# Kernel tuning notes

Hardware: AMD Instinct MI355X
Metric: run time of the kernel (lower is better)

Reference implementation:

```python
import jax, jax.numpy as jnp
import numpy as np

N_NODES = 100000
N_EDGES = 1600000
D_FEAT = 48


def sage_conv(x, src, dst, Wl, Wr, b):
    # mean aggregation of neighbor messages x[src] at dst (PyG source_to_target)
    msg_sum = jax.ops.segment_sum(x[src], dst, num_segments=N_NODES)  # [N, d]
    cnt = jax.ops.segment_sum(jnp.ones((src.shape[0],), x.dtype), dst,
                              num_segments=N_NODES)  # [N]
    mean = msg_sum / jnp.maximum(cnt, 1.0)[:, None]
    # out = lin_l(mean neighbors) + lin_r(self); bias only on lin_l (PyG default)
    return mean @ Wl + b + x @ Wr


def setup_inputs() -> dict:
    key = jax.random.key(0)
    ks = jax.random.split(key, 8)
    x = jax.random.normal(ks[0], (N_NODES, D_FEAT), jnp.float32)
    edge_index = jax.random.randint(ks[1], (2, N_EDGES), 0, N_NODES, jnp.int64)
    def w(k, fi, fo):
        return jax.random.normal(k, (fi, fo), jnp.float32) / np.sqrt(fi)
    return {
        "x": x,
        "edge_index": edge_index,
        "W1l": w(ks[2], D_FEAT, 32), "W1r": w(ks[3], D_FEAT, 32),
        "b1": jnp.zeros((32,), jnp.float32),
        "W2l": w(ks[4], 32, 16), "W2r": w(ks[5], 32, 16),
        "b2": jnp.zeros((16,), jnp.float32),
        "Wlin": w(ks[6], 16, 2), "blin": jnp.zeros((2,), jnp.float32),
    }


def reference(x, edge_index, W1l, W1r, b1, W2l, W2r, b2, Wlin, blin):
    src, dst = edge_index[0], edge_index[1]
    h = jax.nn.relu(sage_conv(x, src, dst, W1l, W1r, b1))
    h = jax.nn.relu(sage_conv(h, src, dst, W2l, W2r, b2))
    return h @ Wlin + blin  # [N, 2] logits
```

## Files before the change

### kernel.cpp

```cpp
#include <hip/hip_runtime.h>
#include <hip/hip_bf16.h>


constexpr int NN  = 100000;
constexpr int NE  = 1600000;
constexpr int NCH = (NN + 255) / 256;
constexpr int NB  = 391;
constexpr int CAP = 4608;
constexpr int SEG = CAP + 3 * 256;
constexpr int T1  = 2048;
constexpr int EPT = T1 / 256;
constexpr int NB1 = (NE + T1 - 1) / T1;

__device__ __forceinline__ float bl(unsigned u) { return __uint_as_float(u << 16); }
__device__ __forceinline__ float bh(unsigned u) { return __uint_as_float(u & 0xffff0000u); }
__device__ __forceinline__ unsigned f2b(float x) {
    unsigned u = __float_as_uint(x);
    return (u + 0x7fffu + ((u >> 16) & 1u)) >> 16;
}
__device__ __forceinline__ unsigned pack2(float a, float b) {
    return f2b(a) | (f2b(b) << 16);
}

__device__ __forceinline__ int wave_incl_scan(int v, int lane) {
#pragma unroll
    for (int d = 1; d < 64; d <<= 1) {
        int t = __shfl_up(v, d, 64);
        if (lane >= d) v += t;
    }
    return v;
}

__global__ __launch_bounds__(256) void k1_kernel(
    const float* __restrict__ X,
    const float* __restrict__ Wl,
    const float* __restrict__ Wr,
    const int*   __restrict__ ei,
    int* __restrict__ bsize, unsigned* __restrict__ bbuf,
    __hip_bfloat16* __restrict__ P, __hip_bfloat16* __restrict__ R)
{
    __shared__ float sW[2][48 * 32];
    __shared__ int hist[NB], base[NB], cur[NB];
    __shared__ int s_any;

    if (blockIdx.x < NCH) {
        for (int i = threadIdx.x; i < 48 * 32; i += 256) {
            sW[0][i] = Wl[i];
            sW[1][i] = Wr[i];
        }
        __syncthreads();
        int n = blockIdx.x * 256 + threadIdx.x;
        if (n > NN) return;
        if (n == NN) {
            uint4 z = make_uint4(0, 0, 0, 0);
            uint4* pp = reinterpret_cast<uint4*>(P + (size_t)NN * 32);
#pragma unroll
            for (int i = 0; i < 4; ++i) pp[i] = z;
            return;
        }
        float xr[48];
        const float4* xp = reinterpret_cast<const float4*>(X + (size_t)n * 48);
#pragma unroll
        for (int i = 0; i < 12; ++i) {
            float4 u = xp[i];
            xr[i*4+0] = u.x; xr[i*4+1] = u.y; xr[i*4+2] = u.z; xr[i*4+3] = u.w;
        }
        float accp[32], accr[32];
#pragma unroll
        for (int j = 0; j < 32; ++j) { accp[j] = 0.f; accr[j] = 0.f; }
#pragma unroll
        for (int k = 0; k < 48; ++k) {
            float xk = xr[k];
#pragma unroll
            for (int j = 0; j < 32; ++j) {
                accp[j] += xk * sW[0][k * 32 + j];
                accr[j] += xk * sW[1][k * 32 + j];
            }
        }
        uint4* pp = reinterpret_cast<uint4*>(P + (size_t)n * 32);
        uint4* rp = reinterpret_cast<uint4*>(R + (size_t)n * 32);
#pragma unroll
        for (int i = 0; i < 4; ++i) {
            uint4 u, v;
            u.x = pack2(accp[i*8+0], accp[i*8+1]); u.y = pack2(accp[i*8+2], accp[i*8+3]);
            u.z = pack2(accp[i*8+4], accp[i*8+5]); u.w = pack2(accp[i*8+6], accp[i*8+7]);
            v.x = pack2(accr[i*8+0], accr[i*8+1]); v.y = pack2(accr[i*8+2], accr[i*8+3]);
            v.z = pack2(accr[i*8+4], accr[i*8+5]); v.w = pack2(accr[i*8+6], accr[i*8+7]);
            pp[i] = u;
            rp[i] = v;
        }
    } else {
        if (threadIdx.x == 0) s_any = 0;
        for (int i = threadIdx.x; i < NB; i += 256) { hist[i] = 0; cur[i] = 0; }
        __syncthreads();
        int dv = 0;
        for (int i = threadIdx.x; i < 2048; i += 256) dv |= ei[2 * i + 1];
        if (dv != 0) atomicOr(&s_any, 1);
        __syncthreads();
        int sh = (s_any == 0) ? 1 : 0;

        int e0 = (blockIdx.x - NCH) * T1;
        int sreg[EPT], dreg[EPT];
#pragma unroll
        for (int it = 0; it < EPT; ++it) {
            int e = e0 + it * 256 + threadIdx.x;
            bool ok = e < NE;
            int s = ok ? ei[(size_t)e << sh] : -1;
            int d = ok ? ei[(size_t)(NE + e) << sh] : -1;
            if ((unsigned)s >= (unsigned)NN || (unsigned)d >= (unsigned)NN) { s = -1; d = -1; }
            sreg[it] = s; dreg[it] = d;
            if (d >= 0) atomicAdd(&hist[d >> 8], 1);
        }
        __syncthreads();
        for (int b = threadIdx.x; b < NB; b += 256) {
            int h = hist[b];
            base[b] = h ? atomicAdd(&bsize[b], h) : 0;
        }
        __syncthreads();
#pragma unroll
        for (int it = 0; it < EPT; ++it) {
            int s = sreg[it], d = dreg[it];
            if (d < 0) continue;
            int b = d >> 8;
            int pos = base[b] + atomicAdd(&cur[b], 1);
            if (pos < CAP)
                bbuf[(size_t)b * CAP + pos] = ((unsigned)s << 8) | (unsigned)(d & 255);
        }
    }
}

__global__ __launch_bounds__(256) void k2_kernel(
    const int* __restrict__ bsize, const unsigned* __restrict__ bbuf,
    int* __restrict__ deg, int* __restrict__ rowstart, int* __restrict__ csr_src)
{
    __shared__ int ldeg[256], lcur[256], ws[4];
    int b = blockIdx.x, t = threadIdx.x;
    int bs = b * SEG;

    int S = min(bsize[b], CAP);
    const unsigned* bp = bbuf + (size_t)b * CAP;
    ldeg[t] = 0;
    __syncthreads();
    for (int i = t; i < S; i += 256)
        atomicAdd(&ldeg[bp[i] & 255u], 1);
    __syncthreads();

    int v  = ldeg[t];
    int pv = (v + 3) & ~3;
    int lane = t & 63, wid = t >> 6;
    int incl = wave_incl_scan(pv, lane);
    if (lane == 63) ws[wid] = incl;
    __syncthreads();
    int off = 0;
#pragma unroll
    for (int w = 0; w < 3; ++w)
        if (wid > w) off += ws[w];
    int excl = off + incl - pv;

    int node = (b << 8) + t;
    if (node < NN) {
        deg[node] = v;
        rowstart[node] = bs + excl;
    }
    lcur[t] = excl;
    __syncthreads();

    for (int i = t; i < S; i += 256) {
        unsigned pk = bp[i];
        int pos = atomicAdd(&lcur[pk & 255u], 1);
        csr_src[bs + pos] = (int)(pk >> 8);
    }
    for (int p = excl + v; p < excl + pv; ++p)
        csr_src[bs + p] = NN;
}

__global__ __launch_bounds__(256) void gather1f_kernel(
    const int* __restrict__ rowstart, const int* __restrict__ deg,
    const int* __restrict__ csr_src,
    const __hip_bfloat16* __restrict__ p1,
    const __hip_bfloat16* __restrict__ r1,
    const float* __restrict__ b1,
    const float* __restrict__ W2l,
    const float* __restrict__ W2r,
    __hip_bfloat16* __restrict__ P2,
    __hip_bfloat16* __restrict__ R2)
{
    __shared__ float sW2l[32 * 16], sW2r[32 * 16], sb1[32];
    __shared__ float shh[32 * 64];
    int t = threadIdx.x;
    for (int i = t; i < 32 * 16; i += 256) { sW2l[i] = W2l[i]; sW2r[i] = W2r[i]; }
    if (t < 32) sb1[t] = b1[t];
    __syncthreads();

    int loc = t >> 2, c = t & 3;
    int n = blockIdx.x * 64 + loc;
    bool valid = n < NN;

    if (valid) {
        int start = rowstart[n], dn = deg[n];
        int pv4 = ((dn + 3) & ~3) >> 2;
        float acc[8];
#pragma unroll
        for (int j = 0; j < 8; ++j) acc[j] = 0.f;
        const uint4* prow = reinterpret_cast<const uint4*>(p1);
        const int4* cp4 = reinterpret_cast<const int4*>(csr_src + start);
        for (int k = 0; k < pv4; ++k) {
            int4 s4 = cp4[k];
            uint4 a = prow[(size_t)s4.x * 4 + c];
            uint4 b = prow[(size_t)s4.y * 4 + c];
            uint4 d = prow[(size_t)s4.z * 4 + c];
            uint4 e = prow[(size_t)s4.w * 4 + c];
            acc[0] += bl(a.x) + bl(b.x) + bl(d.x) + bl(e.x);
            acc[1] += bh(a.x) + bh(b.x) + bh(d.x) + bh(e.x);
            acc[2] += bl(a.y) + bl(b.y) + bl(d.y) + bl(e.y);
            acc[3] += bh(a.y) + bh(b.y) + bh(d.y) + bh(e.y);
            acc[4] += bl(a.z) + bl(b.z) + bl(d.z) + bl(e.z);
            acc[5] += bh(a.z) + bh(b.z) + bh(d.z) + bh(e.z);
            acc[6] += bl(a.w) + bl(b.w) + bl(d.w) + bl(e.w);
            acc[7] += bh(a.w) + bh(b.w) + bh(d.w) + bh(e.w);
        }
        float inv = 1.0f / fmaxf((float)dn, 1.0f);
        uint4 r = reinterpret_cast<const uint4*>(r1)[(size_t)n * 4 + c];
        float rr[8] = { bl(r.x), bh(r.x), bl(r.y), bh(r.y),
                        bl(r.z), bh(r.z), bl(r.w), bh(r.w) };
#pragma unroll
        for (int j = 0; j < 8; ++j)
            shh[(c * 8 + j) * 64 + loc] = fmaxf(acc[j] * inv + rr[j] + sb1[c * 8 + j], 0.f);
    }
    __syncthreads();

    if (valid) {
        float accp[4], accr[4];
#pragma unroll
        for (int j = 0; j < 4; ++j) { accp[j] = 0.f; accr[j] = 0.f; }
#pragma unroll
        for (int k = 0; k < 32; ++k) {
            float hk = shh[k * 64 + loc];
#pragma unroll
            for (int j = 0; j < 4; ++j) {
                accp[j] += hk * sW2l[k * 16 + c * 4 + j];
                accr[j] += hk * sW2r[k * 16 + c * 4 + j];
            }
        }
        uint2 up, ur;
        up.x = pack2(accp[0], accp[1]); up.y = pack2(accp[2], accp[3]);
        ur.x = pack2(accr[0], accr[1]); ur.y = pack2(accr[2], accr[3]);
        reinterpret_cast<uint2*>(P2)[(size_t)n * 4 + c] = up;
        reinterpret_cast<uint2*>(R2)[(size_t)n * 4 + c] = ur;
    } else if (n == NN) {
        uint2 z = make_uint2(0, 0);
        reinterpret_cast<uint2*>(P2)[(size_t)NN * 4 + c] = z;
        reinterpret_cast<uint2*>(R2)[(size_t)NN * 4 + c] = z;
    }
}

__global__ __launch_bounds__(256) void gather2_kernel(
    const int* __restrict__ rowstart, const int* __restrict__ deg,
    const int* __restrict__ csr_src,
    const __hip_bfloat16* __restrict__ P2,
    const __hip_bfloat16* __restrict__ R2,
    const float* __restrict__ b2,
    const float* __restrict__ Wlin,
    const float* __restrict__ blin,
    float* __restrict__ out)
{
    __shared__ float sb[16], sW[32], sbl[2];
    if (threadIdx.x < 16) sb[threadIdx.x] = b2[threadIdx.x];
    else if (threadIdx.x < 48) sW[threadIdx.x - 16] = Wlin[threadIdx.x - 16];
    else if (threadIdx.x < 50) sbl[threadIdx.x - 48] = blin[threadIdx.x - 48];
    __syncthreads();
    int t = blockIdx.x * 256 + threadIdx.x;
    int n = t >> 1, c = t & 1;
    if (n >= NN) return;
    int start = rowstart[n], dn = deg[n];
    int pv4 = ((dn + 3) & ~3) >> 2;

    float acc[8];
#pragma unroll
    for (int j = 0; j < 8; ++j) acc[j] = 0.f;
    const uint4* prow = reinterpret_cast<const uint4*>(P2);
    const int4* cp4 = reinterpret_cast<const int4*>(csr_src + start);
    for (int k = 0; k < pv4; ++k) {
        int4 s4 = cp4[k];
        uint4 a = prow[(size_t)s4.x * 2 + c];
        uint4 b = prow[(size_t)s4.y * 2 + c];
        uint4 d = prow[(size_t)s4.z * 2 + c];
        uint4 e = prow[(size_t)s4.w * 2 + c];
        acc[0] += bl(a.x) + bl(b.x) + bl(d.x) + bl(e.x);
        acc[1] += bh(a.x) + bh(b.x) + bh(d.x) + bh(e.x);
        acc[2] += bl(a.y) + bl(b.y) + bl(d.y) + bl(e.y);
        acc[3] += bh(a.y) + bh(b.y) + bh(d.y) + bh(e.y);
        acc[4] += bl(a.z) + bl(b.z) + bl(d.z) + bl(e.z);
        acc[5] += bh(a.z) + bh(b.z) + bh(d.z) + bh(e.z);
        acc[6] += bl(a.w) + bl(b.w) + bl(d.w) + bl(e.w);
        acc[7] += bh(a.w) + bh(b.w) + bh(d.w) + bh(e.w);
    }
    float inv = 1.0f / fmaxf((float)dn, 1.0f);
    uint4 r = reinterpret_cast<const uint4*>(R2)[(size_t)n * 2 + c];
    float rr[8] = { bl(r.x), bh(r.x), bl(r.y), bh(r.y),
                    bl(r.z), bh(r.z), bl(r.w), bh(r.w) };
    float o0 = 0.f, o1 = 0.f;
#pragma unroll
    for (int j = 0; j < 8; ++j) {
        int kk = c * 8 + j;
        float hv = fmaxf(acc[j] * inv + rr[j] + sb[kk], 0.f);
        o0 += hv * sW[kk * 2];
        o1 += hv * sW[kk * 2 + 1];
    }
    o0 += __shfl_xor(o0, 1, 64);
    o1 += __shfl_xor(o1, 1, 64);
    if (c == 0)
        reinterpret_cast<float2*>(out)[n] = make_float2(o0 + sbl[0], o1 + sbl[1]);
}

extern "C" void kernel_launch(void* const* d_in, const int* in_sizes, int n_in,
                              void* d_out, int out_size, void* d_ws, size_t ws_size,
                              hipStream_t stream)
{
    const float* x    = (const float*)d_in[0];
    const int*   ei   = (const int*)d_in[1];
    const float* W1l  = (const float*)d_in[2];
    const float* W1r  = (const float*)d_in[3];
    const float* b1   = (const float*)d_in[4];
    const float* W2l  = (const float*)d_in[5];
    const float* W2r  = (const float*)d_in[6];
    const float* b2   = (const float*)d_in[7];
    const float* Wlin = (const float*)d_in[8];
    const float* blin = (const float*)d_in[9];
    float* out = (float*)d_out;

    char* wsb = (char*)d_ws;
    int*      bsize    = (int*)(wsb + 64);
    int*      deg      = (int*)(wsb + 4096);
    int*      rowstart = (int*)(wsb + 404096);
    int*      csr_src  = (int*)(wsb + 804096);
    unsigned* bbuf     = (unsigned*)(wsb + 9300000);
    __hip_bfloat16* p1 = (__hip_bfloat16*)(wsb + 16600000);
    __hip_bfloat16* r1 = (__hip_bfloat16*)(wsb + 23100000);
    __hip_bfloat16* p2 = (__hip_bfloat16*)(wsb + 29600000);
    __hip_bfloat16* r2 = (__hip_bfloat16*)(wsb + 32900000);

    dim3 blk(256);

    hipMemsetAsync(bsize, 0, NB * sizeof(int), stream);
    k1_kernel<<<NCH + NB1, blk, 0, stream>>>(x, W1l, W1r, ei, bsize, bbuf, p1, r1);
    k2_kernel<<<NB, blk, 0, stream>>>(bsize, bbuf, deg, rowstart, csr_src);
    gather1f_kernel<<<(NN + 1 + 63) / 64, blk, 0, stream>>>(
        rowstart, deg, csr_src, p1, r1, b1, W2l, W2r, p2, r2);
    gather2_kernel<<<(NN * 2 + 255) / 256, blk, 0, stream>>>(
        rowstart, deg, csr_src, p2, r2, b2, Wlin, blin, out);
}
```

Before: 187.7 us.

## Degree-sort nodes within each bucket to balance gather wave workloads

The CSR build kernel now counts nodes per in-degree value (capped at 63) inside each 256-node bucket and writes a permutation that groups nodes of similar degree together. Both gather kernels read this permutation to decide which node each thread or thread group handles, so lanes in a wave run similar neighbor-loop trip counts. The aim is less wave divergence and idle lanes in the irregular neighbor loops. The cost is an extra histogram, scan and scatter in the CSR build kernel, an extra indirect load per node in the gathers, and output and row accesses that are less sequential within a bucket.

```diff
diff --git a/kernel.cpp b/kernel.cpp
--- a/kernel.cpp
+++ b/kernel.cpp
@@ -11,6 +11,7 @@
 constexpr int T1  = 2048;
 constexpr int EPT = T1 / 256;
 constexpr int NB1 = (NE + T1 - 1) / T1;
+constexpr int NSLOT = NB * 256;
 
 __device__ __forceinline__ float bl(unsigned u) { return __uint_as_float(u << 16); }
 __device__ __forceinline__ float bh(unsigned u) { return __uint_as_float(u & 0xffff0000u); }
@@ -131,15 +132,17 @@
 
 __global__ __launch_bounds__(256) void k2_kernel(
     const int* __restrict__ bsize, const unsigned* __restrict__ bbuf,
-    int* __restrict__ deg, int* __restrict__ rowstart, int* __restrict__ csr_src)
-{
-    __shared__ int ldeg[256], lcur[256], ws[4];
+    int* __restrict__ deg, int* __restrict__ rowstart, int* __restrict__ csr_src,
+    int* __restrict__ perm)
+{
+    __shared__ int ldeg[256], lcur[256], ws[4], phist[64];
     int b = blockIdx.x, t = threadIdx.x;
     int bs = b * SEG;
 
     int S = min(bsize[b], CAP);
     const unsigned* bp = bbuf + (size_t)b * CAP;
     ldeg[t] = 0;
+    if (t < 64) phist[t] = 0;
     __syncthreads();
     for (int i = t; i < S; i += 256)
         atomicAdd(&ldeg[bp[i] & 255u], 1);
@@ -158,12 +161,28 @@
     int excl = off + incl - pv;
 
     int node = (b << 8) + t;
-    if (node < NN) {
+    bool validn = node < NN;
+    if (validn) {
         deg[node] = v;
         rowstart[node] = bs + excl;
     }
     lcur[t] = excl;
-    __syncthreads();
+
+    int bin = min(v, 63);
+    if (validn) atomicAdd(&phist[bin], 1);
+    __syncthreads();
+    if (t < 64) {
+        int c = phist[t];
+        int ip = wave_incl_scan(c, t);
+        phist[t] = ip - c;
+    }
+    __syncthreads();
+    if (validn) {
+        int pos = atomicAdd(&phist[bin], 1);
+        perm[(b << 8) + pos] = node;
+    } else {
+        perm[(b << 8) + t] = node;
+    }
 
     for (int i = t; i < S; i += 256) {
         unsigned pk = bp[i];
@@ -175,6 +194,7 @@
 }
 
 __global__ __launch_bounds__(256) void gather1f_kernel(
+    const int* __restrict__ perm,
     const int* __restrict__ rowstart, const int* __restrict__ deg,
     const int* __restrict__ csr_src,
     const __hip_bfloat16* __restrict__ p1,
@@ -193,7 +213,8 @@
     __syncthreads();
 
     int loc = t >> 2, c = t & 3;
-    int n = blockIdx.x * 64 + loc;
+    int slot = blockIdx.x * 64 + loc;
+    int n = perm[slot];
     bool valid = n < NN;
 
     if (valid) {
@@ -255,6 +276,7 @@
 }
 
 __global__ __launch_bounds__(256) void gather2_kernel(
+    const int* __restrict__ perm,
     const int* __restrict__ rowstart, const int* __restrict__ deg,
     const int* __restrict__ csr_src,
     const __hip_bfloat16* __restrict__ P2,
@@ -270,7 +292,9 @@
     else if (threadIdx.x < 50) sbl[threadIdx.x - 48] = blin[threadIdx.x - 48];
     __syncthreads();
     int t = blockIdx.x * 256 + threadIdx.x;
-    int n = t >> 1, c = t & 1;
+    int slot = t >> 1, c = t & 1;
+    if (slot >= NSLOT) return;
+    int n = perm[slot];
     if (n >= NN) return;
     int start = rowstart[n], dn = deg[n];
     int pv4 = ((dn + 3) & ~3) >> 2;
@@ -333,20 +357,21 @@
     int*      bsize    = (int*)(wsb + 64);
     int*      deg      = (int*)(wsb + 4096);
     int*      rowstart = (int*)(wsb + 404096);
-    int*      csr_src  = (int*)(wsb + 804096);
-    unsigned* bbuf     = (unsigned*)(wsb + 9300000);
-    __hip_bfloat16* p1 = (__hip_bfloat16*)(wsb + 16600000);
-    __hip_bfloat16* r1 = (__hip_bfloat16*)(wsb + 23100000);
-    __hip_bfloat16* p2 = (__hip_bfloat16*)(wsb + 29600000);
-    __hip_bfloat16* r2 = (__hip_bfloat16*)(wsb + 32900000);
+    int*      perm     = (int*)(wsb + 804096);
+    int*      csr_src  = (int*)(wsb + 1300000);
+    unsigned* bbuf     = (unsigned*)(wsb + 9800000);
+    __hip_bfloat16* p1 = (__hip_bfloat16*)(wsb + 17100000);
+    __hip_bfloat16* r1 = (__hip_bfloat16*)(wsb + 23600000);
+    __hip_bfloat16* p2 = (__hip_bfloat16*)(wsb + 30100000);
+    __hip_bfloat16* r2 = (__hip_bfloat16*)(wsb + 33400000);
 
     dim3 blk(256);
 
     hipMemsetAsync(bsize, 0, NB * sizeof(int), stream);
     k1_kernel<<<NCH + NB1, blk, 0, stream>>>(x, W1l, W1r, ei, bsize, bbuf, p1, r1);
-    k2_kernel<<<NB, blk, 0, stream>>>(bsize, bbuf, deg, rowstart, csr_src);
-    gather1f_kernel<<<(NN + 1 + 63) / 64, blk, 0, stream>>>(
-        rowstart, deg, csr_src, p1, r1, b1, W2l, W2r, p2, r2);
-    gather2_kernel<<<(NN * 2 + 255) / 256, blk, 0, stream>>>(
-        rowstart, deg, csr_src, p2, r2, b2, Wlin, blin, out);
-}
+    k2_kernel<<<NB, blk, 0, stream>>>(bsize, bbuf, deg, rowstart, csr_src, perm);
+    gather1f_kernel<<<NSLOT / 64, blk, 0, stream>>>(
+        perm, rowstart, deg, csr_src, p1, r1, b1, W2l, W2r, p2, r2);
+    gather2_kernel<<<(NSLOT * 2 + 255) / 256, blk, 0, stream>>>(
+        perm, rowstart, deg, csr_src, p2, r2, b2, Wlin, blin, out);
+}
```

Result: slower. 207.1 us (+10.4%).
